# Optimization experiments

Hardware: AMD Instinct MI355X
Metric: run time of the kernel (lower is better)

The kernel has to match this reference:

```python
import jax, jax.numpy as jnp
import numpy as np
from jax import lax

N_HEADS = 16
TOP_K = 2
N_EXPERTS = 8

def layer_norm(x, w, b, eps=1e-5):
    mu = jnp.mean(x, axis=-1, keepdims=True)
    var = jnp.mean(jnp.square(x - mu), axis=-1, keepdims=True)
    return (x - mu) * lax.rsqrt(var + eps) * w + b

def attention(x, w_qkv, b_qkv, w_o, b_o):
    B, T, D = x.shape
    dh = D // N_HEADS
    qkv = x @ w_qkv + b_qkv                       # [B,T,3D]
    q, k, v = jnp.split(qkv, 3, axis=-1)
    q = q.reshape(B, T, N_HEADS, dh)
    k = k.reshape(B, T, N_HEADS, dh)
    v = v.reshape(B, T, N_HEADS, dh)
    scores = jnp.einsum('bqhd,bkhd->bhqk', q, k) / jnp.sqrt(jnp.float32(dh)).astype(x.dtype)
    probs = jax.nn.softmax(scores, axis=-1)
    ctx = jnp.einsum('bhqk,bkhd->bqhd', probs, v).reshape(B, T, D)
    return ctx @ w_o + b_o

def moe_ff(x, w_gate, w1, b1, w2, b2):
    # top-k token routing (dropless: equivalent math to gate_and_sort ->
    # dispatch -> grouped expert GEMM -> combine -> unpermute)
    B, T, D = x.shape
    t = x.reshape(B * T, D)                        # [N,D]
    probs = jax.nn.softmax(t @ w_gate, axis=-1)    # [N,E]
    tw, ti = lax.top_k(probs, TOP_K)               # [N,K]
    tw = tw / jnp.sum(tw, axis=-1, keepdims=True)  # renormalize top-k weights
    out = jnp.zeros_like(t)
    for e in range(N_EXPERTS):
        we = jnp.sum(jnp.where(ti == e, tw, 0.0), axis=-1)       # [N]
        h = jax.nn.gelu(t @ w1[e] + b1[e]) @ w2[e] + b2[e]       # expert FFN
        out = out + we[:, None] * h
    return out.reshape(B, T, D)

def reference(x, ln1_w, ln1_b, ln2_w, ln2_b, w_qkv, b_qkv, w_o, b_o, w_gate, w1, b1, w2, b2):
    # pre-norm transformer block: attention then MoE FFN, both residual.
    # The torch module's 2-way micro-batch pipelining is per-token identical
    # to full-batch compute, so we compute the full batch at once.
    h = x + attention(layer_norm(x, ln1_w, ln1_b), w_qkv, b_qkv, w_o, b_o)
    return h + moe_ff(layer_norm(h, ln2_w, ln2_b), w_gate, w1, b1, w2, b2)

def setup_inputs() -> dict:
    key = jax.random.key(0)
    ks = jax.random.split(key, 8)
    B, T, D, H, E = 4, 512, 1024, 4096, 8
    s = lambda d: 1.0 / np.sqrt(d)
    return {
        'x': jax.random.normal(ks[0], (B, T, D), jnp.float32),
        'ln1_w': jnp.ones((D,), jnp.float32),
        'ln1_b': jnp.zeros((D,), jnp.float32),
        'ln2_w': jnp.ones((D,), jnp.float32),
        'ln2_b': jnp.zeros((D,), jnp.float32),
        'w_qkv': jax.random.normal(ks[1], (D, 3 * D), jnp.float32) * s(D),
        'b_qkv': jnp.zeros((3 * D,), jnp.float32),
        'w_o': jax.random.normal(ks[2], (D, D), jnp.float32) * s(D),
        'b_o': jnp.zeros((D,), jnp.float32),
        'w_gate': jax.random.normal(ks[3], (D, E), jnp.float32) * s(D),
        'w1': jax.random.normal(ks[4], (E, D, H), jnp.float32) * s(D),
        'b1': jnp.zeros((E, H), jnp.float32),
        'w2': jax.random.normal(ks[5], (E, H, D), jnp.float32) * s(H),
        'b2': jnp.zeros((E, D), jnp.float32),
    }
```

## Files before the change

kernel.cpp:

```cpp
#include <hip/hip_runtime.h>
#include <math.h>

typedef unsigned short ushort_t;
using short8 = __attribute__((ext_vector_type(8))) short;
using f32x4  = __attribute__((ext_vector_type(4))) float;

#define N_TOK 2048
#define DIM   1024
#define D3    3072
#define NHEAD 16
#define DH    64
#define TT    512
#define HID   4096
#define NEXP  8

__device__ __forceinline__ float bf2f(ushort_t u){
  union { unsigned int i; float f; } x; x.i = ((unsigned int)u) << 16; return x.f;
}
__device__ __forceinline__ ushort_t f2bf(float f){
  union { unsigned int i; float f; } x; x.f = f;
  unsigned int r = x.i + 0x7fffu + ((x.i >> 16) & 1u);
  return (ushort_t)(r >> 16);
}
__device__ __forceinline__ float gelu_f(float x){
  const float c = 0.7978845608028654f;
  float t = tanhf(c * (x + 0.044715f * x * x * x));
  return 0.5f * x * (1.0f + t);
}

template<int MODE>
__global__ __launch_bounds__(256) void ln_k(const float* __restrict__ xin,
                                            const float* __restrict__ w,
                                            const float* __restrict__ b,
                                            float* __restrict__ out,
                                            ushort_t* __restrict__ outhi,
                                            ushort_t* __restrict__ outlo){
  int tok = blockIdx.x;
  int t = threadIdx.x;
  float vals[4]; float s = 0.f, ss = 0.f;
#pragma unroll
  for (int i = 0; i < 4; i++){
    int d = t + i * 256;
    float v = xin[(size_t)tok * DIM + d];
    vals[i] = v; s += v; ss += v * v;
  }
  __shared__ float rs[256], rq[256];
  rs[t] = s; rq[t] = ss; __syncthreads();
  for (int k = 128; k > 0; k >>= 1){
    if (t < k){ rs[t] += rs[t + k]; rq[t] += rq[t + k]; }
    __syncthreads();
  }
  float mu  = rs[0] * (1.0f / DIM);
  float var = rq[0] * (1.0f / DIM) - mu * mu;
  float inv = rsqrtf(var + 1e-5f);
#pragma unroll
  for (int i = 0; i < 4; i++){
    int d = t + i * 256;
    float r = (vals[i] - mu) * inv * w[d] + b[d];
    size_t idx = (size_t)tok * DIM + d;
    if (MODE == 1){
      out[idx] = r;
      outhi[idx] = f2bf(r);
    } else {
      ushort_t hv = f2bf(r);
      outhi[idx] = hv;
      outlo[idx] = f2bf(r - bf2f(hv));
    }
  }
}

__global__ __launch_bounds__(256) void convT2(const float* __restrict__ src,
                                              ushort_t* __restrict__ dhi,
                                              ushort_t* __restrict__ dlo,
                                              int R, int C){
  __shared__ float tile[64][65];
  int r0 = blockIdx.y * 64, c0 = blockIdx.x * 64;
  int t = threadIdx.x;
  int tc = t & 15, tr = t >> 4;
#pragma unroll
  for (int i = 0; i < 4; i++){
    int r = tr + i * 16;
    float4 v = *(const float4*)&src[(size_t)(r0 + r) * C + c0 + tc * 4];
    tile[r][tc*4 + 0] = v.x; tile[r][tc*4 + 1] = v.y;
    tile[r][tc*4 + 2] = v.z; tile[r][tc*4 + 3] = v.w;
  }
  __syncthreads();
#pragma unroll
  for (int i = 0; i < 4; i++){
    int c = tr + i * 16;
    float v0 = tile[tc*4 + 0][c];
    float v1 = tile[tc*4 + 1][c];
    float v2 = tile[tc*4 + 2][c];
    float v3 = tile[tc*4 + 3][c];
    ushort4 oh, ol;
    oh.x = f2bf(v0); ol.x = f2bf(v0 - bf2f(oh.x));
    oh.y = f2bf(v1); ol.y = f2bf(v1 - bf2f(oh.y));
    oh.z = f2bf(v2); ol.z = f2bf(v2 - bf2f(oh.z));
    oh.w = f2bf(v3); ol.w = f2bf(v3 - bf2f(oh.w));
    size_t o = (size_t)(c0 + c) * R + r0 + tc * 4;
    *(ushort4*)&dhi[o] = oh;
    *(ushort4*)&dlo[o] = ol;
  }
}

__global__ __launch_bounds__(256) void convT_g(const float* __restrict__ src0,
                                               ushort_t* __restrict__ dst0,
                                               int R, int C){
  size_t eo = (size_t)blockIdx.z * R * C;
  const float* src = src0 + eo;
  ushort_t* dst = dst0 + eo;
  __shared__ float tile[64][65];
  int r0 = blockIdx.y * 64, c0 = blockIdx.x * 64;
  int t = threadIdx.x;
  int tc = t & 15, tr = t >> 4;
#pragma unroll
  for (int i = 0; i < 4; i++){
    int r = tr + i * 16;
    float4 v = *(const float4*)&src[(size_t)(r0 + r) * C + c0 + tc * 4];
    tile[r][tc*4 + 0] = v.x; tile[r][tc*4 + 1] = v.y;
    tile[r][tc*4 + 2] = v.z; tile[r][tc*4 + 3] = v.w;
  }
  __syncthreads();
#pragma unroll
  for (int i = 0; i < 4; i++){
    int c = tr + i * 16;
    ushort4 o;
    o.x = f2bf(tile[tc*4 + 0][c]);
    o.y = f2bf(tile[tc*4 + 1][c]);
    o.z = f2bf(tile[tc*4 + 2][c]);
    o.w = f2bf(tile[tc*4 + 3][c]);
    *(ushort4*)&dst[(size_t)(c0 + c) * R + r0 + tc * 4] = o;
  }
}

#define TBM 128
#define TBN 128
#define TBK 32
#define LDK 40

template<int EPI>
__global__ __launch_bounds__(256) void gemm_split(
    const ushort_t* __restrict__ Ahi, const ushort_t* __restrict__ Alo,
    const ushort_t* __restrict__ Bhi, const ushort_t* __restrict__ Blo,
    const float* __restrict__ bias,
    float* __restrict__ C, const float* __restrict__ Res,
    int Nn, int K, int mblocks)
{
  int q = gridDim.x >> 3;
  int L = (blockIdx.x & 7) * q + (blockIdx.x >> 3);
  int bm = (L % mblocks) * TBM;
  int bn = (L / mblocks) * TBN;
  __shared__ ushort_t Ah[TBM * LDK];
  __shared__ ushort_t Al[TBM * LDK];
  __shared__ ushort_t Bh[TBN * LDK];
  __shared__ ushort_t Bl[TBN * LDK];
  int t = threadIdx.x;
  int lane = t & 63, wave = t >> 6;
  int wm = (wave & 1) * 64, wn = (wave >> 1) * 64;

  int r0 = t >> 2, r1 = r0 + 64;
  int kc = (t & 3) * 8;
  const ushort_t* ah0 = Ahi + (size_t)(bm + r0) * K + kc;
  const ushort_t* ah1 = Ahi + (size_t)(bm + r1) * K + kc;
  const ushort_t* al0 = Alo + (size_t)(bm + r0) * K + kc;
  const ushort_t* al1 = Alo + (size_t)(bm + r1) * K + kc;
  const ushort_t* bh0 = Bhi + (size_t)(bn + r0) * K + kc;
  const ushort_t* bh1 = Bhi + (size_t)(bn + r1) * K + kc;
  const ushort_t* bl0 = Blo + (size_t)(bn + r0) * K + kc;
  const ushort_t* bl1 = Blo + (size_t)(bn + r1) * K + kc;

  f32x4 acc[4][4] = {};
  int fm = lane & 15, fk = (lane >> 4) * 8;

  uint4 vah0 = *(const uint4*)(ah0);
  uint4 vah1 = *(const uint4*)(ah1);
  uint4 val0 = *(const uint4*)(al0);
  uint4 val1 = *(const uint4*)(al1);
  uint4 vbh0 = *(const uint4*)(bh0);
  uint4 vbh1 = *(const uint4*)(bh1);
  uint4 vbl0 = *(const uint4*)(bl0);
  uint4 vbl1 = *(const uint4*)(bl1);

  for (int k0 = 0; k0 < K; k0 += TBK){
    *(uint4*)&Ah[r0 * LDK + kc] = vah0;
    *(uint4*)&Ah[r1 * LDK + kc] = vah1;
    *(uint4*)&Al[r0 * LDK + kc] = val0;
    *(uint4*)&Al[r1 * LDK + kc] = val1;
    *(uint4*)&Bh[r0 * LDK + kc] = vbh0;
    *(uint4*)&Bh[r1 * LDK + kc] = vbh1;
    *(uint4*)&Bl[r0 * LDK + kc] = vbl0;
    *(uint4*)&Bl[r1 * LDK + kc] = vbl1;
    __syncthreads();
    int kn = k0 + TBK;
    if (kn < K){
      vah0 = *(const uint4*)(ah0 + kn);
      vah1 = *(const uint4*)(ah1 + kn);
      val0 = *(const uint4*)(al0 + kn);
      val1 = *(const uint4*)(al1 + kn);
      vbh0 = *(const uint4*)(bh0 + kn);
      vbh1 = *(const uint4*)(bh1 + kn);
      vbl0 = *(const uint4*)(bl0 + kn);
      vbl1 = *(const uint4*)(bl1 + kn);
    }
    short8 afh[4], afl[4], bfh[4], bfl[4];
#pragma unroll
    for (int mi = 0; mi < 4; mi++){
      afh[mi] = *(const short8*)&Ah[(wm + mi*16 + fm) * LDK + fk];
      afl[mi] = *(const short8*)&Al[(wm + mi*16 + fm) * LDK + fk];
    }
#pragma unroll
    for (int nj = 0; nj < 4; nj++){
      bfh[nj] = *(const short8*)&Bh[(wn + nj*16 + fm) * LDK + fk];
      bfl[nj] = *(const short8*)&Bl[(wn + nj*16 + fm) * LDK + fk];
    }
#pragma unroll
    for (int mi = 0; mi < 4; mi++)
#pragma unroll
      for (int nj = 0; nj < 4; nj++){
        acc[mi][nj] = __builtin_amdgcn_mfma_f32_16x16x32_bf16(afh[mi], bfh[nj], acc[mi][nj], 0, 0, 0);
        acc[mi][nj] = __builtin_amdgcn_mfma_f32_16x16x32_bf16(afh[mi], bfl[nj], acc[mi][nj], 0, 0, 0);
        acc[mi][nj] = __builtin_amdgcn_mfma_f32_16x16x32_bf16(afl[mi], bfh[nj], acc[mi][nj], 0, 0, 0);
      }
    __syncthreads();
  }

#pragma unroll
  for (int mi = 0; mi < 4; mi++){
    int rowbase = bm + wm + mi*16 + (lane >> 4) * 4;
#pragma unroll
    for (int nj = 0; nj < 4; nj++){
      int n = bn + wn + nj*16 + (lane & 15);
      f32x4 v = acc[mi][nj];
#pragma unroll
      for (int rg = 0; rg < 4; rg++){
        size_t idx = (size_t)(rowbase + rg) * Nn + n;
        float val = v[rg] + bias[n];
        if (EPI == 1) val += Res[idx];
        C[idx] = val;
      }
    }
  }
}

__global__ __launch_bounds__(256) void scores_k(const float* __restrict__ qkv,
                                                float* __restrict__ S){
  int bh = blockIdx.z; int b = bh >> 4, h = bh & 15;
  int q0 = blockIdx.y * 64, k0 = blockIdx.x * 64;
  __shared__ float Qs[64][68];
  __shared__ float Ks[64][68];
  int t = threadIdx.x;
  int r = t >> 2, dp = (t & 3) * 16;
  {
    const float* qp = qkv + (size_t)(b * TT + q0 + r) * D3 + h * DH + dp;
    const float* kp = qkv + (size_t)(b * TT + k0 + r) * D3 + DIM + h * DH + dp;
#pragma unroll
    for (int c = 0; c < 4; c++){
      float4 qv = *(const float4*)(qp + c * 4);
      float4 kv = *(const float4*)(kp + c * 4);
      Qs[dp + c*4 + 0][r] = qv.x; Qs[dp + c*4 + 1][r] = qv.y;
      Qs[dp + c*4 + 2][r] = qv.z; Qs[dp + c*4 + 3][r] = qv.w;
      Ks[dp + c*4 + 0][r] = kv.x; Ks[dp + c*4 + 1][r] = kv.y;
      Ks[dp + c*4 + 2][r] = kv.z; Ks[dp + c*4 + 3][r] = kv.w;
    }
  }
  __syncthreads();
  int tx = t & 15, ty = t >> 4;
  float acc[4][4] = {};
#pragma unroll 8
  for (int d = 0; d < 64; d++){
    float4 qv = *(const float4*)&Qs[d][ty * 4];
    float4 kv = *(const float4*)&Ks[d][tx * 4];
    float qa[4] = {qv.x,qv.y,qv.z,qv.w};
    float ka[4] = {kv.x,kv.y,kv.z,kv.w};
#pragma unroll
    for (int i = 0; i < 4; i++)
#pragma unroll
      for (int j = 0; j < 4; j++)
        acc[i][j] += qa[i] * ka[j];
  }
#pragma unroll
  for (int i = 0; i < 4; i++)
#pragma unroll
    for (int j = 0; j < 4; j++)
      S[((size_t)bh * TT + q0 + ty*4 + i) * TT + k0 + tx*4 + j] = acc[i][j] * 0.125f;
}

__global__ __launch_bounds__(256) void softmax_k(float* __restrict__ S){
  size_t row = blockIdx.x;
  float* p = S + row * TT;
  int t = threadIdx.x;
  float v0 = p[t], v1 = p[t + 256];
  __shared__ float red[256];
  red[t] = fmaxf(v0, v1); __syncthreads();
  for (int k = 128; k > 0; k >>= 1){ if (t < k) red[t] = fmaxf(red[t], red[t + k]); __syncthreads(); }
  float m = red[0]; __syncthreads();
  float e0 = expf(v0 - m), e1 = expf(v1 - m);
  red[t] = e0 + e1; __syncthreads();
  for (int k = 128; k > 0; k >>= 1){ if (t < k) red[t] += red[t + k]; __syncthreads(); }
  float inv = 1.0f / red[0];
  p[t] = e0 * inv; p[t + 256] = e1 * inv;
}

__global__ __launch_bounds__(256) void ctx_k(const float* __restrict__ P,
                                             const float* __restrict__ qkv,
                                             ushort_t* __restrict__ chi,
                                             ushort_t* __restrict__ clo){
  int bh = blockIdx.y; int b = bh >> 4, h = bh & 15;
  int q0 = blockIdx.x * 64;
  __shared__ float Ps[16][68];
  __shared__ float Vs[16][68];
  int t = threadIdx.x;
  int tx = t & 15, ty = t >> 4;
  int pq = t >> 2, pk = (t & 3) * 4;
  int vk = t >> 4, vd = (t & 15) * 4;
  float acc[4][4] = {};
  for (int kk = 0; kk < TT; kk += 16){
    float4 pv = *(const float4*)&P[((size_t)bh * TT + q0 + pq) * TT + kk + pk];
    Ps[pk + 0][pq] = pv.x; Ps[pk + 1][pq] = pv.y;
    Ps[pk + 2][pq] = pv.z; Ps[pk + 3][pq] = pv.w;
    float4 vv = *(const float4*)&qkv[(size_t)(b * TT + kk + vk) * D3 + 2 * DIM + h * DH + vd];
    Vs[vk][vd + 0] = vv.x; Vs[vk][vd + 1] = vv.y;
    Vs[vk][vd + 2] = vv.z; Vs[vk][vd + 3] = vv.w;
    __syncthreads();
#pragma unroll
    for (int k = 0; k < 16; k++){
      float4 a = *(const float4*)&Ps[k][ty * 4];
      float4 bb = *(const float4*)&Vs[k][tx * 4];
      float aa[4] = {a.x,a.y,a.z,a.w};
      float bv[4] = {bb.x,bb.y,bb.z,bb.w};
#pragma unroll
      for (int i = 0; i < 4; i++)
#pragma unroll
        for (int j = 0; j < 4; j++)
          acc[i][j] += aa[i] * bv[j];
    }
    __syncthreads();
  }
#pragma unroll
  for (int i = 0; i < 4; i++)
#pragma unroll
    for (int j = 0; j < 4; j++){
      float v = acc[i][j];
      size_t idx = (size_t)(b * TT + q0 + ty*4 + i) * DIM + h * DH + tx*4 + j;
      ushort_t hv = f2bf(v);
      chi[idx] = hv;
      clo[idx] = f2bf(v - bf2f(hv));
    }
}

__global__ __launch_bounds__(256) void gate_k(const float* __restrict__ ln2f,
                                              const float* __restrict__ wg,
                                              float* __restrict__ we){
  int tok = blockIdx.x * 4 + (threadIdx.x >> 6);
  int lane = threadIdx.x & 63;
  float acc[8] = {};
  for (int d = lane; d < DIM; d += 64){
    float x = ln2f[(size_t)tok * DIM + d];
    float4 w0 = *(const float4*)&wg[d * 8];
    float4 w1v = *(const float4*)&wg[d * 8 + 4];
    float wv[8] = {w0.x,w0.y,w0.z,w0.w,w1v.x,w1v.y,w1v.z,w1v.w};
#pragma unroll
    for (int e = 0; e < 8; e++) acc[e] += x * wv[e];
  }
#pragma unroll
  for (int off = 32; off > 0; off >>= 1){
#pragma unroll
    for (int e = 0; e < 8; e++) acc[e] += __shfl_down(acc[e], off);
  }
  if (lane == 0){
    float m = acc[0];
    for (int e = 1; e < 8; e++) m = fmaxf(m, acc[e]);
    float pr[8], s = 0.f;
    for (int e = 0; e < 8; e++){ pr[e] = expf(acc[e] - m); s += pr[e]; }
    for (int e = 0; e < 8; e++) pr[e] /= s;
    int i0 = 0;
    for (int e = 1; e < 8; e++) if (pr[e] > pr[i0]) i0 = e;
    int i1 = (i0 == 0) ? 1 : 0;
    for (int e = 0; e < 8; e++) if (e != i0 && pr[e] > pr[i1]) i1 = e;
    float sm = pr[i0] + pr[i1];
    for (int e = 0; e < 8; e++)
      we[(size_t)tok * 8 + e] = (e == i0) ? pr[i0] / sm : ((e == i1) ? pr[i1] / sm : 0.f);
  }
}

__global__ __launch_bounds__(256) void route_k(const float* __restrict__ we,
                                               int* __restrict__ cnt,
                                               int* __restrict__ gidx,
                                               float* __restrict__ gw){
  int tok = blockIdx.x * 256 + threadIdx.x;
#pragma unroll
  for (int e = 0; e < NEXP; e++){
    float w = we[(size_t)tok * NEXP + e];
    if (w > 0.f){
      int p = atomicAdd(&cnt[e], 1);
      gidx[e * N_TOK + p] = tok;
      gw[e * N_TOK + p] = w;
    }
  }
}

__global__ void plan_k(const int* __restrict__ cnt, int* __restrict__ off,
                       int* __restrict__ table){
  if (threadIdx.x == 0){
    int s = 0;
    for (int e = 0; e < NEXP; e++){ off[e] = s; s += cnt[e]; }
    int ns = 0;
    for (int e = 0; e < NEXP; e++){
      int nb = (cnt[e] + TBM - 1) / TBM;
      for (int rb = 0; rb < nb; rb++) table[1 + ns++] = (e << 16) | rb;
    }
    table[0] = ns;
  }
}

template<int EPI>
__global__ __launch_bounds__(256) void moe_gemm_g(
    const ushort_t* __restrict__ A,
    const ushort_t* __restrict__ BT_all,
    const float* __restrict__ bias_all,
    ushort_t* __restrict__ Obf,
    float* __restrict__ Of,
    const int* __restrict__ gidx_all,
    const float* __restrict__ gw_all,
    const int* __restrict__ cnt,
    const int* __restrict__ off,
    const int* __restrict__ table,
    int Nn)
{
  int ns = table[0];
  int slot = blockIdx.y;
  if (slot >= ns) return;
  int ent = table[1 + slot];
  int e  = ent >> 16;
  int bm = (ent & 0xffff) * TBM;
  int c  = cnt[e];
  int col, ks;
  if (EPI == 0){ col = blockIdx.x; ks = 0; }
  else         { col = blockIdx.x & 7; ks = blockIdx.x >> 3; }
  const int K = (EPI == 0) ? DIM : HID;
  int kbase = ks * 1024;
  int bn = col * TBN;
  const int* gidx = gidx_all + e * N_TOK;
  const float* gwp = gw_all + e * N_TOK;
  const ushort_t* BT = BT_all + (size_t)e * Nn * K;
  const float* bias = bias_all + (size_t)e * Nn;
  int obase = off[e];

  __shared__ ushort_t As[TBM * LDK];
  __shared__ ushort_t Bs[TBN * LDK];
  int t = threadIdx.x;
  int lane = t & 63, wave = t >> 6;
  int wm = (wave & 1) * 64, wn = (wave >> 1) * 64;

  int r0 = t >> 2, r1 = r0 + 64;
  int kc = (t & 3) * 8;
  size_t ga0, ga1;
  if (EPI == 0){
    int g0 = bm + r0, g1 = bm + r1;
    ga0 = (size_t)((g0 < c) ? gidx[g0] : gidx[bm]);
    ga1 = (size_t)((g1 < c) ? gidx[g1] : gidx[bm]);
  } else {
    int mx = 2 * N_TOK - 1;
    int g0 = obase + bm + r0; if (g0 > mx) g0 = mx;
    int g1 = obase + bm + r1; if (g1 > mx) g1 = mx;
    ga0 = (size_t)g0; ga1 = (size_t)g1;
  }
  const ushort_t* a0p = A + ga0 * K + kbase + kc;
  const ushort_t* a1p = A + ga1 * K + kbase + kc;
  const ushort_t* b0p = BT + (size_t)(bn + r0) * K + kbase + kc;
  const ushort_t* b1p = BT + (size_t)(bn + r1) * K + kbase + kc;

  f32x4 acc[4][4] = {};
  int fm = lane & 15, fk = (lane >> 4) * 8;

  uint4 Aa0 = *(const uint4*)(a0p);
  uint4 Aa1 = *(const uint4*)(a1p);
  uint4 Ba0 = *(const uint4*)(b0p);
  uint4 Ba1 = *(const uint4*)(b1p);
  uint4 Ab0 = *(const uint4*)(a0p + TBK);
  uint4 Ab1 = *(const uint4*)(a1p + TBK);
  uint4 Bb0 = *(const uint4*)(b0p + TBK);
  uint4 Bb1 = *(const uint4*)(b1p + TBK);

  const int KSTEPS = 32;
  for (int it = 0; it < KSTEPS; it += 2){
    *(uint4*)&As[r0 * LDK + kc] = Aa0;
    *(uint4*)&As[r1 * LDK + kc] = Aa1;
    *(uint4*)&Bs[r0 * LDK + kc] = Ba0;
    *(uint4*)&Bs[r1 * LDK + kc] = Ba1;
    __syncthreads();
    if (it + 2 < KSTEPS){
      int kn = (it + 2) * TBK;
      Aa0 = *(const uint4*)(a0p + kn);
      Aa1 = *(const uint4*)(a1p + kn);
      Ba0 = *(const uint4*)(b0p + kn);
      Ba1 = *(const uint4*)(b1p + kn);
    }
    {
      short8 af[4], bfr[4];
#pragma unroll
      for (int mi = 0; mi < 4; mi++)
        af[mi] = *(const short8*)&As[(wm + mi*16 + fm) * LDK + fk];
#pragma unroll
      for (int nj = 0; nj < 4; nj++)
        bfr[nj] = *(const short8*)&Bs[(wn + nj*16 + fm) * LDK + fk];
#pragma unroll
      for (int mi = 0; mi < 4; mi++)
#pragma unroll
        for (int nj = 0; nj < 4; nj++)
          acc[mi][nj] = __builtin_amdgcn_mfma_f32_16x16x32_bf16(af[mi], bfr[nj], acc[mi][nj], 0, 0, 0);
    }
    __syncthreads();
    *(uint4*)&As[r0 * LDK + kc] = Ab0;
    *(uint4*)&As[r1 * LDK + kc] = Ab1;
    *(uint4*)&Bs[r0 * LDK + kc] = Bb0;
    *(uint4*)&Bs[r1 * LDK + kc] = Bb1;
    __syncthreads();
    if (it + 3 < KSTEPS){
      int kn = (it + 3) * TBK;
      Ab0 = *(const uint4*)(a0p + kn);
      Ab1 = *(const uint4*)(a1p + kn);
      Bb0 = *(const uint4*)(b0p + kn);
      Bb1 = *(const uint4*)(b1p + kn);
    }
    {
      short8 af[4], bfr[4];
#pragma unroll
      for (int mi = 0; mi < 4; mi++)
        af[mi] = *(const short8*)&As[(wm + mi*16 + fm) * LDK + fk];
#pragma unroll
      for (int nj = 0; nj < 4; nj++)
        bfr[nj] = *(const short8*)&Bs[(wn + nj*16 + fm) * LDK + fk];
#pragma unroll
      for (int mi = 0; mi < 4; mi++)
#pragma unroll
        for (int nj = 0; nj < 4; nj++)
          acc[mi][nj] = __builtin_amdgcn_mfma_f32_16x16x32_bf16(af[mi], bfr[nj], acc[mi][nj], 0, 0, 0);
    }
    __syncthreads();
  }

#pragma unroll
  for (int mi = 0; mi < 4; mi++){
    int rowbase = bm + wm + mi*16 + (lane >> 4) * 4;
#pragma unroll
    for (int nj = 0; nj < 4; nj++){
      int n = bn + wn + nj*16 + (lane & 15);
      f32x4 v = acc[mi][nj];
#pragma unroll
      for (int rg = 0; rg < 4; rg++){
        int r = rowbase + rg;
        if (r < c){
          if (EPI == 0){
            float val = v[rg] + bias[n];
            Obf[(size_t)(obase + r) * Nn + n] = f2bf(gelu_f(val));
          } else {
            float val = v[rg];
            if (ks == 0) val += bias[n];
            int tok = gidx[r];
            atomicAdd(&Of[(size_t)tok * Nn + n], gwp[r] * val);
          }
        }
      }
    }
  }
}

__global__ __launch_bounds__(256) void final_k(const float* __restrict__ h,
                                               const float* __restrict__ acc,
                                               float* __restrict__ out){
  size_t i = (size_t)blockIdx.x * 256 + threadIdx.x;
  out[i] = h[i] + acc[i];
}

extern "C" void kernel_launch(void* const* d_in, const int* in_sizes, int n_in,
                              void* d_out, int out_size, void* d_ws, size_t ws_size,
                              hipStream_t stream){
  const float* x     = (const float*)d_in[0];
  const float* ln1w  = (const float*)d_in[1];
  const float* ln1b  = (const float*)d_in[2];
  const float* ln2w  = (const float*)d_in[3];
  const float* ln2b  = (const float*)d_in[4];
  const float* wqkv  = (const float*)d_in[5];
  const float* bqkv  = (const float*)d_in[6];
  const float* wo    = (const float*)d_in[7];
  const float* bo    = (const float*)d_in[8];
  const float* wgate = (const float*)d_in[9];
  const float* w1    = (const float*)d_in[10];
  const float* b1    = (const float*)d_in[11];
  const float* w2    = (const float*)d_in[12];
  const float* b2    = (const float*)d_in[13];

  char* ws = (char*)d_ws;
  const size_t MB = 1024 * 1024;
  float*    hbuf  = (float*)(ws + 0 * MB);
  ushort_t* ln1hi = (ushort_t*)(ws + 0 * MB);
  ushort_t* ln1lo = (ushort_t*)(ws + 4 * MB);
  float*    accb  = (float*)(ws + 8 * MB);
  ushort_t* wqkvThi = (ushort_t*)(ws + 8 * MB);
  ushort_t* wqkvTlo = (ushort_t*)(ws + 14 * MB);
  ushort_t* ln2bf = (ushort_t*)(ws + 16 * MB);
  ushort_t* h1e   = (ushort_t*)(ws + 20 * MB);
  float*    qkv   = (float*)(ws + 20 * MB);
  float*    ln2f  = (float*)(ws + 24 * MB);
  ushort_t* ctxhi = (ushort_t*)(ws + 44 * MB);
  ushort_t* ctxlo = (ushort_t*)(ws + 48 * MB);
  ushort_t* woThi = (ushort_t*)(ws + 52 * MB);
  ushort_t* woTlo = (ushort_t*)(ws + 54 * MB);
  float*    sc    = (float*)(ws + 56 * MB);
  ushort_t* wTe   = (ushort_t*)(ws + 56 * MB);
  float*    webuf = (float*)(ws + 120 * MB);
  int*      cnt   = (int*)  (ws + 120 * MB + 256 * 1024);
  int*      off   = (int*)  (ws + 120 * MB + 260 * 1024);
  int*      table = (int*)  (ws + 120 * MB + 264 * 1024);
  int*      bidx  = (int*)  (ws + 120 * MB + 320 * 1024);
  float*    bw    = (float*)(ws + 120 * MB + 448 * 1024);

  ln_k<2><<<N_TOK, 256, 0, stream>>>(x, ln1w, ln1b, nullptr, ln1hi, ln1lo);
  convT2<<<dim3(D3 / 64, DIM / 64), 256, 0, stream>>>(wqkv, wqkvThi, wqkvTlo, DIM, D3);
  gemm_split<0><<<(N_TOK / TBM) * (D3 / TBN), 256, 0, stream>>>(
      ln1hi, ln1lo, wqkvThi, wqkvTlo, bqkv, qkv, nullptr, D3, DIM, N_TOK / TBM);
  scores_k<<<dim3(8, 8, 64), 256, 0, stream>>>(qkv, sc);
  softmax_k<<<64 * TT, 256, 0, stream>>>(sc);
  ctx_k<<<dim3(8, 64), 256, 0, stream>>>(sc, qkv, ctxhi, ctxlo);
  convT_g<<<dim3(HID / 64, DIM / 64, NEXP), 256, 0, stream>>>(w1, wTe, DIM, HID);
  convT2<<<dim3(DIM / 64, DIM / 64), 256, 0, stream>>>(wo, woThi, woTlo, DIM, DIM);
  gemm_split<1><<<(N_TOK / TBM) * (DIM / TBN), 256, 0, stream>>>(
      ctxhi, ctxlo, woThi, woTlo, bo, hbuf, x, DIM, DIM, N_TOK / TBM);
  ln_k<1><<<N_TOK, 256, 0, stream>>>(hbuf, ln2w, ln2b, ln2f, ln2bf, nullptr);
  gate_k<<<N_TOK / 4, 256, 0, stream>>>(ln2f, wgate, webuf);

  hipMemsetAsync(cnt, 0, 32, stream);
  hipMemsetAsync(accb, 0, (size_t)N_TOK * DIM * 4, stream);
  route_k<<<N_TOK / 256, 256, 0, stream>>>(webuf, cnt, bidx, bw);
  plan_k<<<1, 64, 0, stream>>>(cnt, off, table);
  moe_gemm_g<0><<<dim3(HID / TBN, 40), 256, 0, stream>>>(
      ln2bf, wTe, b1, h1e, nullptr, bidx, bw, cnt, off, table, HID);
  convT_g<<<dim3(DIM / 64, HID / 64, NEXP), 256, 0, stream>>>(w2, wTe, HID, DIM);
  moe_gemm_g<1><<<dim3(32, 40), 256, 0, stream>>>(
      h1e, wTe, b2, nullptr, accb, bidx, bw, cnt, off, table, DIM);
  final_k<<<(N_TOK * DIM) / 256, 256, 0, stream>>>(hbuf, accb, (float*)d_out);
}
```

Baseline: 823.1 us.

## Use direct global-to-LDS loads in split and grouped expert GEMMs

Replaces register-staged global loads plus LDS stores with __builtin_amdgcn_global_load_lds 16-byte transfers in both the split-precision GEMM and the MoE grouped GEMM. The LDS row stride drops from 40 to 32 elements with no padding, and the staging layout is reassigned per wave. The aim is to cut VGPR pressure and the extra LDS write instructions. In exchange, the register prefetch that overlapped the next tile's loads with MFMA work is gone, the unpadded layout may cause LDS bank conflicts on fragment reads, and there is no explicit vmcnt wait before the barrier.

```diff
diff --git a/kernel.cpp b/kernel.cpp
--- a/kernel.cpp
+++ b/kernel.cpp
@@ -26,6 +26,9 @@
   const float c = 0.7978845608028654f;
   float t = tanhf(c * (x + 0.044715f * x * x * x));
   return 0.5f * x * (1.0f + t);
+}
+__device__ __forceinline__ void gload16(const ushort_t* g, ushort_t* l){
+  __builtin_amdgcn_global_load_lds((const unsigned int*)g, (unsigned int*)l, 16, 0, 0);
 }
 
 template<int MODE>
@@ -136,7 +139,7 @@
 #define TBM 128
 #define TBN 128
 #define TBK 32
-#define LDK 40
+#define LDB 32
 
 template<int EPI>
 __global__ __launch_bounds__(256) void gemm_split(
@@ -150,68 +153,53 @@
   int L = (blockIdx.x & 7) * q + (blockIdx.x >> 3);
   int bm = (L % mblocks) * TBM;
   int bn = (L / mblocks) * TBN;
-  __shared__ ushort_t Ah[TBM * LDK];
-  __shared__ ushort_t Al[TBM * LDK];
-  __shared__ ushort_t Bh[TBN * LDK];
-  __shared__ ushort_t Bl[TBN * LDK];
+  __shared__ ushort_t Ah[TBM * LDB];
+  __shared__ ushort_t Al[TBM * LDB];
+  __shared__ ushort_t Bh[TBN * LDB];
+  __shared__ ushort_t Bl[TBN * LDB];
   int t = threadIdx.x;
   int lane = t & 63, wave = t >> 6;
   int wm = (wave & 1) * 64, wn = (wave >> 1) * 64;
 
-  int r0 = t >> 2, r1 = r0 + 64;
-  int kc = (t & 3) * 8;
-  const ushort_t* ah0 = Ahi + (size_t)(bm + r0) * K + kc;
-  const ushort_t* ah1 = Ahi + (size_t)(bm + r1) * K + kc;
-  const ushort_t* al0 = Alo + (size_t)(bm + r0) * K + kc;
-  const ushort_t* al1 = Alo + (size_t)(bm + r1) * K + kc;
-  const ushort_t* bh0 = Bhi + (size_t)(bn + r0) * K + kc;
-  const ushort_t* bh1 = Bhi + (size_t)(bn + r1) * K + kc;
-  const ushort_t* bl0 = Blo + (size_t)(bn + r0) * K + kc;
-  const ushort_t* bl1 = Blo + (size_t)(bn + r1) * K + kc;
+  int sr0 = wave * 32 + (lane >> 2);
+  int sr1 = sr0 + 16;
+  int sc  = (lane & 3) * 8;
+  const ushort_t* ah0 = Ahi + (size_t)(bm + sr0) * K + sc;
+  const ushort_t* ah1 = Ahi + (size_t)(bm + sr1) * K + sc;
+  const ushort_t* al0 = Alo + (size_t)(bm + sr0) * K + sc;
+  const ushort_t* al1 = Alo + (size_t)(bm + sr1) * K + sc;
+  const ushort_t* bh0 = Bhi + (size_t)(bn + sr0) * K + sc;
+  const ushort_t* bh1 = Bhi + (size_t)(bn + sr1) * K + sc;
+  const ushort_t* bl0 = Blo + (size_t)(bn + sr0) * K + sc;
+  const ushort_t* bl1 = Blo + (size_t)(bn + sr1) * K + sc;
+  ushort_t* lAh0 = Ah + (wave * 32) * LDB;
+  ushort_t* lAh1 = Ah + (wave * 32 + 16) * LDB;
+  ushort_t* lAl0 = Al + (wave * 32) * LDB;
+  ushort_t* lAl1 = Al + (wave * 32 + 16) * LDB;
+  ushort_t* lBh0 = Bh + (wave * 32) * LDB;
+  ushort_t* lBh1 = Bh + (wave * 32 + 16) * LDB;
+  ushort_t* lBl0 = Bl + (wave * 32) * LDB;
+  ushort_t* lBl1 = Bl + (wave * 32 + 16) * LDB;
 
   f32x4 acc[4][4] = {};
   int fm = lane & 15, fk = (lane >> 4) * 8;
 
-  uint4 vah0 = *(const uint4*)(ah0);
-  uint4 vah1 = *(const uint4*)(ah1);
-  uint4 val0 = *(const uint4*)(al0);
-  uint4 val1 = *(const uint4*)(al1);
-  uint4 vbh0 = *(const uint4*)(bh0);
-  uint4 vbh1 = *(const uint4*)(bh1);
-  uint4 vbl0 = *(const uint4*)(bl0);
-  uint4 vbl1 = *(const uint4*)(bl1);
-
   for (int k0 = 0; k0 < K; k0 += TBK){
-    *(uint4*)&Ah[r0 * LDK + kc] = vah0;
-    *(uint4*)&Ah[r1 * LDK + kc] = vah1;
-    *(uint4*)&Al[r0 * LDK + kc] = val0;
-    *(uint4*)&Al[r1 * LDK + kc] = val1;
-    *(uint4*)&Bh[r0 * LDK + kc] = vbh0;
-    *(uint4*)&Bh[r1 * LDK + kc] = vbh1;
-    *(uint4*)&Bl[r0 * LDK + kc] = vbl0;
-    *(uint4*)&Bl[r1 * LDK + kc] = vbl1;
-    __syncthreads();
-    int kn = k0 + TBK;
-    if (kn < K){
-      vah0 = *(const uint4*)(ah0 + kn);
-      vah1 = *(const uint4*)(ah1 + kn);
-      val0 = *(const uint4*)(al0 + kn);
-      val1 = *(const uint4*)(al1 + kn);
-      vbh0 = *(const uint4*)(bh0 + kn);
-      vbh1 = *(const uint4*)(bh1 + kn);
-      vbl0 = *(const uint4*)(bl0 + kn);
-      vbl1 = *(const uint4*)(bl1 + kn);
-    }
+    gload16(ah0 + k0, lAh0); gload16(ah1 + k0, lAh1);
+    gload16(al0 + k0, lAl0); gload16(al1 + k0, lAl1);
+    gload16(bh0 + k0, lBh0); gload16(bh1 + k0, lBh1);
+    gload16(bl0 + k0, lBl0); gload16(bl1 + k0, lBl1);
+    __syncthreads();
     short8 afh[4], afl[4], bfh[4], bfl[4];
 #pragma unroll
     for (int mi = 0; mi < 4; mi++){
-      afh[mi] = *(const short8*)&Ah[(wm + mi*16 + fm) * LDK + fk];
-      afl[mi] = *(const short8*)&Al[(wm + mi*16 + fm) * LDK + fk];
+      afh[mi] = *(const short8*)&Ah[(wm + mi*16 + fm) * LDB + fk];
+      afl[mi] = *(const short8*)&Al[(wm + mi*16 + fm) * LDB + fk];
     }
 #pragma unroll
     for (int nj = 0; nj < 4; nj++){
-      bfh[nj] = *(const short8*)&Bh[(wn + nj*16 + fm) * LDK + fk];
-      bfl[nj] = *(const short8*)&Bl[(wn + nj*16 + fm) * LDK + fk];
+      bfh[nj] = *(const short8*)&Bh[(wn + nj*16 + fm) * LDB + fk];
+      bfl[nj] = *(const short8*)&Bl[(wn + nj*16 + fm) * LDB + fk];
     }
 #pragma unroll
     for (int mi = 0; mi < 4; mi++)
@@ -446,97 +434,56 @@
   const float* bias = bias_all + (size_t)e * Nn;
   int obase = off[e];
 
-  __shared__ ushort_t As[TBM * LDK];
-  __shared__ ushort_t Bs[TBN * LDK];
+  __shared__ ushort_t As[TBM * LDB];
+  __shared__ ushort_t Bs[TBN * LDB];
   int t = threadIdx.x;
   int lane = t & 63, wave = t >> 6;
   int wm = (wave & 1) * 64, wn = (wave >> 1) * 64;
 
-  int r0 = t >> 2, r1 = r0 + 64;
-  int kc = (t & 3) * 8;
+  int sr0 = wave * 32 + (lane >> 2);
+  int sr1 = sr0 + 16;
+  int sc  = (lane & 3) * 8;
   size_t ga0, ga1;
   if (EPI == 0){
-    int g0 = bm + r0, g1 = bm + r1;
+    int g0 = bm + sr0, g1 = bm + sr1;
     ga0 = (size_t)((g0 < c) ? gidx[g0] : gidx[bm]);
     ga1 = (size_t)((g1 < c) ? gidx[g1] : gidx[bm]);
   } else {
     int mx = 2 * N_TOK - 1;
-    int g0 = obase + bm + r0; if (g0 > mx) g0 = mx;
-    int g1 = obase + bm + r1; if (g1 > mx) g1 = mx;
+    int g0 = obase + bm + sr0; if (g0 > mx) g0 = mx;
+    int g1 = obase + bm + sr1; if (g1 > mx) g1 = mx;
     ga0 = (size_t)g0; ga1 = (size_t)g1;
   }
-  const ushort_t* a0p = A + ga0 * K + kbase + kc;
-  const ushort_t* a1p = A + ga1 * K + kbase + kc;
-  const ushort_t* b0p = BT + (size_t)(bn + r0) * K + kbase + kc;
-  const ushort_t* b1p = BT + (size_t)(bn + r1) * K + kbase + kc;
+  const ushort_t* a0p = A + ga0 * K + kbase + sc;
+  const ushort_t* a1p = A + ga1 * K + kbase + sc;
+  const ushort_t* b0p = BT + (size_t)(bn + sr0) * K + kbase + sc;
+  const ushort_t* b1p = BT + (size_t)(bn + sr1) * K + kbase + sc;
+  ushort_t* lA0 = As + (wave * 32) * LDB;
+  ushort_t* lA1 = As + (wave * 32 + 16) * LDB;
+  ushort_t* lB0 = Bs + (wave * 32) * LDB;
+  ushort_t* lB1 = Bs + (wave * 32 + 16) * LDB;
 
   f32x4 acc[4][4] = {};
   int fm = lane & 15, fk = (lane >> 4) * 8;
 
-  uint4 Aa0 = *(const uint4*)(a0p);
-  uint4 Aa1 = *(const uint4*)(a1p);
-  uint4 Ba0 = *(const uint4*)(b0p);
-  uint4 Ba1 = *(const uint4*)(b1p);
-  uint4 Ab0 = *(const uint4*)(a0p + TBK);
-  uint4 Ab1 = *(const uint4*)(a1p + TBK);
-  uint4 Bb0 = *(const uint4*)(b0p + TBK);
-  uint4 Bb1 = *(const uint4*)(b1p + TBK);
-
-  const int KSTEPS = 32;
-  for (int it = 0; it < KSTEPS; it += 2){
-    *(uint4*)&As[r0 * LDK + kc] = Aa0;
-    *(uint4*)&As[r1 * LDK + kc] = Aa1;
-    *(uint4*)&Bs[r0 * LDK + kc] = Ba0;
-    *(uint4*)&Bs[r1 * LDK + kc] = Ba1;
-    __syncthreads();
-    if (it + 2 < KSTEPS){
-      int kn = (it + 2) * TBK;
-      Aa0 = *(const uint4*)(a0p + kn);
-      Aa1 = *(const uint4*)(a1p + kn);
-      Ba0 = *(const uint4*)(b0p + kn);
-      Ba1 = *(const uint4*)(b1p + kn);
-    }
-    {
-      short8 af[4], bfr[4];
-#pragma unroll
-      for (int mi = 0; mi < 4; mi++)
-        af[mi] = *(const short8*)&As[(wm + mi*16 + fm) * LDK + fk];
+  for (int k0 = 0; k0 < 1024; k0 += TBK){
+    gload16(a0p + k0, lA0);
+    gload16(a1p + k0, lA1);
+    gload16(b0p + k0, lB0);
+    gload16(b1p + k0, lB1);
+    __syncthreads();
+    short8 af[4], bfr[4];
+#pragma unroll
+    for (int mi = 0; mi < 4; mi++)
+      af[mi] = *(const short8*)&As[(wm + mi*16 + fm) * LDB + fk];
+#pragma unroll
+    for (int nj = 0; nj < 4; nj++)
+      bfr[nj] = *(const short8*)&Bs[(wn + nj*16 + fm) * LDB + fk];
+#pragma unroll
+    for (int mi = 0; mi < 4; mi++)
 #pragma unroll
       for (int nj = 0; nj < 4; nj++)
-        bfr[nj] = *(const short8*)&Bs[(wn + nj*16 + fm) * LDK + fk];
-#pragma unroll
-      for (int mi = 0; mi < 4; mi++)
-#pragma unroll
-        for (int nj = 0; nj < 4; nj++)
-          acc[mi][nj] = __builtin_amdgcn_mfma_f32_16x16x32_bf16(af[mi], bfr[nj], acc[mi][nj], 0, 0, 0);
-    }
-    __syncthreads();
-    *(uint4*)&As[r0 * LDK + kc] = Ab0;
-    *(uint4*)&As[r1 * LDK + kc] = Ab1;
-    *(uint4*)&Bs[r0 * LDK + kc] = Bb0;
-    *(uint4*)&Bs[r1 * LDK + kc] = Bb1;
-    __syncthreads();
-    if (it + 3 < KSTEPS){
-      int kn = (it + 3) * TBK;
-      Ab0 = *(const uint4*)(a0p + kn);
-      Ab1 = *(const uint4*)(a1p + kn);
-      Bb0 = *(const uint4*)(b0p + kn);
-      Bb1 = *(const uint4*)(b1p + kn);
-    }
-    {
-      short8 af[4], bfr[4];
-#pragma unroll
-      for (int mi = 0; mi < 4; mi++)
-        af[mi] = *(const short8*)&As[(wm + mi*16 + fm) * LDK + fk];
-#pragma unroll
-      for (int nj = 0; nj < 4; nj++)
-        bfr[nj] = *(const short8*)&Bs[(wn + nj*16 + fm) * LDK + fk];
-#pragma unroll
-      for (int mi = 0; mi < 4; mi++)
-#pragma unroll
-        for (int nj = 0; nj < 4; nj++)
-          acc[mi][nj] = __builtin_amdgcn_mfma_f32_16x16x32_bf16(af[mi], bfr[nj], acc[mi][nj], 0, 0, 0);
-    }
+        acc[mi][nj] = __builtin_amdgcn_mfma_f32_16x16x32_bf16(af[mi], bfr[nj], acc[mi][nj], 0, 0, 0);
     __syncthreads();
   }
 
```

Measured after the change: 810.7 us. Within noise of the previous version (-1.5%).
